# Optimization experiments

Hardware: AMD Instinct MI355X
Metric: run time of the kernel (lower is better)

The kernel has to match this reference:

```python
import jax, jax.numpy as jnp
import numpy as np
import math

EPS = 1e-5
NUM_HEADS = 8

def _ln(x, g, b):
    m = x.mean(-1, keepdims=True)
    v = ((x - m) ** 2).mean(-1, keepdims=True)
    return (x - m) / jnp.sqrt(v + EPS) * g + b

def _swish(x):
    return x * jax.nn.sigmoid(x)

def _rope(x):
    # lucidrains RotaryEmbedding.rotate_queries_or_keys: rotates along axis -2,
    # interleaved pair convention, base 10000.
    n, d = x.shape[-2], x.shape[-1]
    inv = 1.0 / (10000.0 ** (jnp.arange(0, d, 2, dtype=jnp.float32) / d))
    freqs = jnp.arange(n, dtype=jnp.float32)[:, None] * inv[None, :]  # (n, d/2)
    cos = jnp.repeat(jnp.cos(freqs), 2, axis=-1)  # (n, d)
    sin = jnp.repeat(jnp.sin(freqs), 2, axis=-1)
    x1, x2 = x[..., 0::2], x[..., 1::2]
    rot = jnp.stack([-x2, x1], axis=-1).reshape(x.shape)
    return x * cos + rot * sin

def _ffn(x, w1, b1, w2, b2):
    # FeedForwardModule: x + 0.5 * (Linear -> Swish -> Linear)
    return x + 0.5 * (_swish(x @ w1 + b1) @ w2 + b2)

def _mhsa(x, g, b, wq, bq, wk, bk, wv, bv, wo, bo):
    B, T, D = x.shape
    dh = D // NUM_HEADS
    y = _ln(x, g, b)
    q = (y @ wq + bq).reshape(B, T, NUM_HEADS, dh)                         # (b,t,h,d)
    k = (y @ wk + bk).reshape(B, T, NUM_HEADS, dh).transpose(0, 2, 1, 3)   # (b,h,t,d)
    v = (y @ wv + bv).reshape(B, T, NUM_HEADS, dh).transpose(0, 2, 1, 3)
    # Faithful to source: query is NOT permuted before rotary, so RoPE acts on
    # axis -2 which is heads for q and time for k (matches torch code exactly).
    q = _rope(q).transpose(0, 2, 1, 3)                                     # (b,h,t,d)
    k = _rope(k)
    score = jnp.einsum('bhtd,bhsd->bhts', q, k) / math.sqrt(D)             # /sqrt(d_model)
    attn = jax.nn.softmax(score, axis=-1)
    ctx = jnp.einsum('bhts,bhsd->bhtd', attn, v).transpose(0, 2, 1, 3).reshape(B, T, D)
    return x + ctx @ wo + bo

def _conv_module(x, g, b, pw1_w, pw1_b, dw_w, dw_b, bn_g, bn_b, pw2_w, pw2_b):
    C = dw_w.shape[-1]  # 2*dim
    y = _ln(x, g, b)
    y = jnp.einsum('btd,ed->bte', y, pw1_w) + pw1_b            # pointwise conv (b,t,4*dim)
    a, gate = y[..., :C], y[..., C:]
    y = a * jax.nn.sigmoid(gate)                                # GLU over channel dim
    y = jax.lax.conv_general_dilated(
        y, dw_w, window_strides=(1,), padding='SAME',
        dimension_numbers=('NWC', 'WIO', 'NWC'), feature_group_count=C) + dw_b
    m = y.mean(axis=(0, 1))                                     # BatchNorm1d, training stats
    v = ((y - m) ** 2).mean(axis=(0, 1))
    y = (y - m) / jnp.sqrt(v + EPS) * bn_g + bn_b
    y = _swish(y)
    y = jnp.einsum('btc,dc->btd', y, pw2_w) + pw2_b             # pointwise conv back to dim
    return x + y

def setup_inputs():
    key = jax.random.key(0)
    B, T, D, K = 8, 1024, 512, 31
    HID = 2 * D
    C = 2 * D
    ks = jax.random.split(key, 16)
    rn = lambda k, shp: jax.random.normal(k, shp, jnp.float32) * 0.02
    zeros = lambda n: jnp.zeros((n,), jnp.float32)
    ones = lambda n: jnp.ones((n,), jnp.float32)
    return dict(
        x=jax.random.normal(ks[0], (B, T, D), jnp.float32),
        ffn1_w1=rn(ks[1], (D, HID)), ffn1_b1=zeros(HID),
        ffn1_w2=rn(ks[2], (HID, D)), ffn1_b2=zeros(D),
        ln_attn_g=ones(D), ln_attn_b=zeros(D),
        wq=rn(ks[3], (D, D)), bq=zeros(D),
        wk=rn(ks[4], (D, D)), bk=zeros(D),
        wv=rn(ks[5], (D, D)), bv=zeros(D),
        wo=rn(ks[6], (D, D)), bo=zeros(D),
        conv_ln_g=ones(D), conv_ln_b=zeros(D),
        pw1_w=rn(ks[7], (2 * C, D)), pw1_b=zeros(2 * C),
        dw_w=rn(ks[8], (K, 1, C)), dw_b=zeros(C),
        bn_g=ones(C), bn_b=zeros(C),
        pw2_w=rn(ks[9], (D, C)), pw2_b=zeros(D),
        ffn2_w1=rn(ks[10], (D, HID)), ffn2_b1=zeros(HID),
        ffn2_w2=rn(ks[11], (HID, D)), ffn2_b2=zeros(D),
        ln_out_g=ones(D), ln_out_b=zeros(D),
    )

def reference(x, ffn1_w1, ffn1_b1, ffn1_w2, ffn1_b2, ln_attn_g, ln_attn_b,
              wq, bq, wk, bk, wv, bv, wo, bo,
              conv_ln_g, conv_ln_b, pw1_w, pw1_b, dw_w, dw_b, bn_g, bn_b, pw2_w, pw2_b,
              ffn2_w1, ffn2_b1, ffn2_w2, ffn2_b2, ln_out_g, ln_out_b):
    y = _ffn(x, ffn1_w1, ffn1_b1, ffn1_w2, ffn1_b2)
    y = _mhsa(y, ln_attn_g, ln_attn_b, wq, bq, wk, bk, wv, bv, wo, bo)
    y = _conv_module(y, conv_ln_g, conv_ln_b, pw1_w, pw1_b, dw_w, dw_b, bn_g, bn_b, pw2_w, pw2_b)
    y = _ffn(y, ffn2_w1, ffn2_b1, ffn2_w2, ffn2_b2)
    return _ln(y, ln_out_g, ln_out_b)
```

## Files before the change

### kernel.cpp

```cpp
#include <hip/hip_runtime.h>
#include <hip/hip_bf16.h>


#define M_ROWS 8192

using bf16x8 = __attribute__((ext_vector_type(8))) short;
using f32x4  = __attribute__((ext_vector_type(4))) float;
using s8v    = __attribute__((ext_vector_type(8))) short;
using s4v    = __attribute__((ext_vector_type(4))) short;

__device__ __forceinline__ float sigmoid_(float v) { return 1.f / (1.f + expf(-v)); }

__device__ __forceinline__ float bf2f(short s) {
  return __uint_as_float(((unsigned)(unsigned short)s) << 16);
}
__device__ __forceinline__ short f2bf(float f) {
  __hip_bfloat16 h = __float2bfloat16(f);
  return *reinterpret_cast<short*>(&h);
}

__device__ __forceinline__ void gl16(const void* g, void* l) {
  __builtin_amdgcn_global_load_lds((const __attribute__((address_space(1))) void*)g,
                                   (__attribute__((address_space(3))) void*)l, 16, 0, 0);
}

template <int BM, int BN, int BK, int EPI, int THREADS>
__global__ __launch_bounds__(THREADS) void mgemm(
    const short* __restrict__ A, const short* __restrict__ Bt,
    const float* __restrict__ bias, const float* __restrict__ res,
    const short* __restrict__ resb, short* __restrict__ outb, int M, int N, int K) {
  constexpr int NW = THREADS / 64;
  constexpr int WR = BM / 64;
  constexpr int WC = NW / WR;
  constexpr int NF = BN / (16 * WC);
  constexpr int CPW = BN / WC;
  constexpr int KH = BK / 32;
  constexpr int RPP = THREADS / (BK / 8);
  constexpr int APASS = BM / RPP;
  constexpr int BPASS = BN / RPP;
  constexpr int LPS = APASS + BPASS;
  __shared__ __align__(16) short smem[2 * BM * BK + 2 * BN * BK];
  short* As0 = smem;
  short* Bs0 = smem + 2 * BM * BK;
  const int tid = threadIdx.x;
  const int lane = tid & 63, wid = tid >> 6;
  const int wr = wid / WC, wc = wid % WC;
  const int nbx = gridDim.x;
  const int nwg = nbx * gridDim.y;
  int id = blockIdx.y * nbx + blockIdx.x;
  id = (id & 7) * (nwg >> 3) + (id >> 3);
  const int bm = (id / nbx) * BM;
  const int bn = (id % nbx) * BN;
  f32x4 acc[4][NF];
#pragma unroll
  for (int m = 0; m < 4; ++m)
#pragma unroll
    for (int n = 0; n < NF; ++n) acc[m][n] = (f32x4){0.f, 0.f, 0.f, 0.f};
  const short* Ablk = A + (size_t)bm * K;
  const short* Bblk = Bt + (size_t)bn * K;
  const int jl = tid & (BK / 8 - 1);
  const int r0 = tid / (BK / 8);
  const int ks = ((BK == 64) ? (jl ^ (r0 & 7)) : jl) << 3;
#define STAGE(buf, k0)                                                                 \
  do {                                                                                 \
    _Pragma("unroll")                                                                  \
    for (int p = 0; p < APASS; ++p)                                                    \
      gl16(Ablk + (size_t)(r0 + p * RPP) * K + (k0) + ks,                              \
           (char*)(As0 + (buf) * BM * BK) + p * (THREADS * 16) + wid * 1024);          \
    _Pragma("unroll")                                                                  \
    for (int p = 0; p < BPASS; ++p)                                                    \
      gl16(Bblk + (size_t)(r0 + p * RPP) * K + (k0) + ks,                              \
           (char*)(Bs0 + (buf) * BN * BK) + p * (THREADS * 16) + wid * 1024);          \
  } while (0)

  STAGE(0, 0);
  STAGE(1, BK);
  const int NS = K / BK;
  const int fr = lane & 15, fg = lane >> 4;
  const int arow = wr * 64 + fr;
  const int brow = wc * CPW + fr;
  for (int i = 0; i < NS; ++i) {
    if (i + 1 < NS) {
      if constexpr (LPS == 6)      asm volatile("s_waitcnt vmcnt(6)" ::: "memory");
      else if constexpr (LPS == 4) asm volatile("s_waitcnt vmcnt(4)" ::: "memory");
      else if constexpr (LPS == 3) asm volatile("s_waitcnt vmcnt(3)" ::: "memory");
      else                         asm volatile("s_waitcnt vmcnt(2)" ::: "memory");
    } else {
      asm volatile("s_waitcnt vmcnt(0)" ::: "memory");
    }
    __builtin_amdgcn_s_barrier();
    asm volatile("" ::: "memory");
    const int cur = i & 1;
    bf16x8 af[KH][4], bfr[KH][NF];
#pragma unroll
    for (int kk = 0; kk < KH; ++kk) {
      const int cx = (BK == 64) ? (((((kk << 2) + fg)) ^ (fr & 7)) << 3)
                                : ((fg << 3) + kk * 32);
#pragma unroll
      for (int m = 0; m < 4; ++m)
        af[kk][m] = *reinterpret_cast<const bf16x8*>(
            &As0[cur * BM * BK + (arow + m * 16) * BK + cx]);
#pragma unroll
      for (int n = 0; n < NF; ++n)
        bfr[kk][n] = *reinterpret_cast<const bf16x8*>(
            &Bs0[cur * BN * BK + (brow + n * 16) * BK + cx]);
    }
    asm volatile("s_waitcnt lgkmcnt(0)" ::: "memory");
    __builtin_amdgcn_s_barrier();
    if ((i + 2) * BK < K) STAGE(cur, (i + 2) * BK);
#pragma unroll
    for (int kk = 0; kk < KH; ++kk)
#pragma unroll
      for (int m = 0; m < 4; ++m)
#pragma unroll
        for (int n = 0; n < NF; ++n)
          acc[m][n] = __builtin_amdgcn_mfma_f32_16x16x32_bf16(af[kk][m], bfr[kk][n],
                                                              acc[m][n], 0, 0, 0);
  }
#undef STAGE
  const int orow0 = bm + wr * 64 + ((lane >> 4) << 2);
  const int ocol0 = bn + wc * CPW + fr;

  if constexpr (EPI == 4) {
    const int sel = bn >> 9;
    const float2* tbl = (const float2*)res;
    if (sel == 2) {
      short* vstg = smem;
      const int b_ = bm >> 10, t0v = bm & 1023;
      const int hb = (bn & 511) >> 6;
#pragma unroll
      for (int pass = 0; pass < 2; ++pass) {
        __syncthreads();
        if (((wc * CPW) >> 6) == pass) {
          const int dlb = (wc * CPW) & 63;
#pragma unroll
          for (int m = 0; m < 4; ++m) {
            const int rl = wr * 64 + ((lane >> 4) << 2) + m * 16;
#pragma unroll
            for (int n = 0; n < NF; ++n) {
              const int dl = dlb + n * 16 + fr;
              const float bv = bias[bn + pass * 64 + dl];
#pragma unroll
              for (int r = 0; r < 4; ++r)
                vstg[dl * 132 + rl + r] = f2bf(acc[m][n][r] + bv);
            }
          }
        }
        __syncthreads();
        for (int c = tid; c < 1024; c += THREADS) {
          const int d = c >> 4, t8 = (c & 15) << 3;
          const s8v val = *reinterpret_cast<const s8v*>(&vstg[d * 132 + t8]);
          *reinterpret_cast<s8v*>(
              &outb[(size_t)8388608 + (((size_t)((b_ << 3) + hb + pass)) << 16) +
                    ((size_t)d << 10) + t0v + t8]) = val;
        }
      }
    } else {
      const float qsc = (sel == 0) ? 0.04419417382415922f : 1.f;
#pragma unroll
      for (int n = 0; n < NF; ++n) {
        const int col = ocol0 + n * 16;
        const int h = (col >> 6) & 7, d = col & 63;
        const int p = d >> 1;
        const float bv = bias[col];
#pragma unroll
        for (int m = 0; m < 4; ++m) {
#pragma unroll
          for (int r = 0; r < 4; ++r) {
            const int row = orow0 + m * 16 + r;
            const int b_ = row >> 10, t_ = row & 1023;
            const int pos = (sel == 0) ? h : t_;
            const float2 cs = tbl[pos * 32 + p];
            float vv = acc[m][n][r] + bv;
            const float pv = __shfl_xor(vv, 1);
            float o = ((lane & 1) == 0) ? (vv * cs.x - pv * cs.y) : (vv * cs.x + pv * cs.y);
            outb[(size_t)sel * 4194304 + (((size_t)((b_ << 3) + h)) << 16) + ((size_t)t_ << 6) + d] =
                f2bf(o * qsc);
          }
        }
      }
    }
  } else if constexpr (EPI == 6) {
#pragma unroll
    for (int m = 0; m < 4; ++m) {
#pragma unroll
      for (int np = 0; np < NF / 2; ++np) {
        const int colbase = bn + wc * CPW + ((2 * np) << 4);
        const int j = colbase >> 7;
        const int u = (colbase >> 5) & 3;
        const int gc = (j << 6) + (u << 4) + fr;
        const float ba = bias[gc];
        const float bg = bias[1024 + gc];
#pragma unroll
        for (int r = 0; r < 4; ++r) {
          const int row = orow0 + m * 16 + r;
          const float a = acc[m][2 * np][r] + ba;
          const float g = acc[m][2 * np + 1][r] + bg;
          outb[(size_t)row * 1024 + gc] = f2bf(a * sigmoid_(g));
        }
      }
    }
  } else {
#pragma unroll
    for (int m = 0; m < 4; ++m) {
#pragma unroll
      for (int n = 0; n < NF; ++n) {
        const int col = ocol0 + n * 16;
        const float bv = bias[col];
#pragma unroll
        for (int r = 0; r < 4; ++r) {
          const int row = orow0 + m * 16 + r;
          float v = acc[m][n][r] + bv;
          if constexpr (EPI == 1) {
            v = v * sigmoid_(v);
          } else if constexpr (EPI == 2) {
            v += bf2f(resb[(size_t)row * N + col]);
          } else if constexpr (EPI == 3) {
            v = bf2f(resb[(size_t)row * N + col]) + 0.5f * v;
          }
          outb[(size_t)row * N + col] = f2bf(v);
        }
      }
    }
  }
}

__device__ __forceinline__ void dev_cast8(const float* in, short* out, int i) {
  const float4 a = *reinterpret_cast<const float4*>(&in[(size_t)i * 8]);
  const float4 b = *reinterpret_cast<const float4*>(&in[(size_t)i * 8 + 4]);
  s8v o = { f2bf(a.x), f2bf(a.y), f2bf(a.z), f2bf(a.w),
            f2bf(b.x), f2bf(b.y), f2bf(b.z), f2bf(b.w) };
  *reinterpret_cast<s8v*>(&out[(size_t)i * 8]) = o;
}

__global__ __launch_bounds__(256) void prep_kernel(
    const float* __restrict__ x, short* __restrict__ xb,
    const float* __restrict__ f1w1, short* __restrict__ wf1w1,
    const float* __restrict__ f1w2, short* __restrict__ wf1w2,
    const float* __restrict__ wq, const float* __restrict__ wk,
    const float* __restrict__ wv, short* __restrict__ wqkv,
    const float* __restrict__ wo, short* __restrict__ wwo,
    const float* __restrict__ pw1, short* __restrict__ wpw1,
    const float* __restrict__ pw2, short* __restrict__ wpw2,
    const float* __restrict__ f2w1, short* __restrict__ wf2w1,
    const float* __restrict__ f2w2, short* __restrict__ wf2w2,
    const float* __restrict__ bq, const float* __restrict__ bk,
    const float* __restrict__ bv, float* __restrict__ bqkv,
    float* __restrict__ rtbl) {
  __shared__ float t[32][33];
  const int blk = blockIdx.x, tid = threadIdx.x;
  const float* tin = nullptr;
  short* tout = nullptr;
  int tK = 0, tN = 0, tr = 0, tnbx = 0;
  if (blk < 2048) {
    dev_cast8(x, xb, blk * 256 + tid);
    return;
  } else if (blk < 2560) { tin = f1w1; tout = wf1w1; tK = 512; tN = 1024; tr = blk - 2048; tnbx = 32; }
  else if (blk < 3072)   { tin = f1w2; tout = wf1w2; tK = 1024; tN = 512; tr = blk - 2560; tnbx = 16; }
  else if (blk < 3328)   { tin = wq; tout = wqkv; tK = 512; tN = 512; tr = blk - 3072; tnbx = 16; }
  else if (blk < 3584)   { tin = wk; tout = wqkv + 512 * 512; tK = 512; tN = 512; tr = blk - 3328; tnbx = 16; }
  else if (blk < 3840)   { tin = wv; tout = wqkv + 1024 * 512; tK = 512; tN = 512; tr = blk - 3584; tnbx = 16; }
  else if (blk < 4096)   { tin = wo; tout = wwo; tK = 512; tN = 512; tr = blk - 3840; tnbx = 16; }
  else if (blk < 4608) {
    const int idx = (blk - 4096) * 256 + tid;
    const int pc = idx >> 6, kk = (idx & 63) << 3;
    const int j = pc >> 7, s = (pc >> 4) & 7, fr = pc & 15;
    const int oc = ((s & 1) << 10) + (j << 6) + ((s >> 1) << 4) + fr;
    const float4 a = *reinterpret_cast<const float4*>(&pw1[(size_t)oc * 512 + kk]);
    const float4 b = *reinterpret_cast<const float4*>(&pw1[(size_t)oc * 512 + kk + 4]);
    s8v o = { f2bf(a.x), f2bf(a.y), f2bf(a.z), f2bf(a.w),
              f2bf(b.x), f2bf(b.y), f2bf(b.z), f2bf(b.w) };
    *reinterpret_cast<s8v*>(&wpw1[(size_t)pc * 512 + kk]) = o;
    return;
  } else if (blk < 4864) {
    dev_cast8(pw2, wpw2, (blk - 4608) * 256 + tid);
    return;
  } else if (blk < 5376) { tin = f2w1; tout = wf2w1; tK = 512; tN = 1024; tr = blk - 4864; tnbx = 32; }
  else if (blk < 5888)   { tin = f2w2; tout = wf2w2; tK = 1024; tN = 512; tr = blk - 5376; tnbx = 16; }
  else if (blk < 6016) {
    const int i = (blk - 5888) * 256 + tid;
    const int tt = i >> 5, p = i & 31;
    const float inv = exp2f(-(float)p * 0.41524101186092f);
    float s, c;
    sincosf((float)tt * inv, &s, &c);
    rtbl[i * 2] = c;
    rtbl[i * 2 + 1] = s;
    return;
  } else {
    const int i = (blk - 6016) * 256 + tid;
    if (i < 1536) bqkv[i] = i < 512 ? bq[i] : (i < 1024 ? bk[i - 512] : bv[i - 1024]);
    return;
  }
  const int n0 = (tr % tnbx) << 5, k0 = (tr / tnbx) << 5;
  const int tx = tid & 31, ty = tid >> 5;
  for (int r = ty; r < 32; r += 8) t[r][tx] = tin[(size_t)(k0 + r) * tN + n0 + tx];
  __syncthreads();
  for (int r = ty; r < 32; r += 8) tout[(size_t)(n0 + r) * tK + k0 + tx] = f2bf(t[tx][r]);
}

template <typename OT>
__global__ __launch_bounds__(256) void ln_kernel(
    const short* __restrict__ in, const float* __restrict__ g,
    const float* __restrict__ b, OT* __restrict__ out) {
  const int tid = threadIdx.x, lane = tid & 63;
  const size_t row = ((size_t)blockIdx.x << 2) + (tid >> 6);
  const int c0 = lane << 3;
  const s8v v = *reinterpret_cast<const s8v*>(&in[(row << 9) + c0]);
  float f[8];
  float s = 0.f;
#pragma unroll
  for (int j = 0; j < 8; ++j) { f[j] = bf2f(v[j]); s += f[j]; }
  for (int o = 32; o; o >>= 1) s += __shfl_xor(s, o);
  const float mean = s * (1.f / 512.f);
  float d[8];
  float q = 0.f;
#pragma unroll
  for (int j = 0; j < 8; ++j) { d[j] = f[j] - mean; q = fmaf(d[j], d[j], q); }
  for (int o = 32; o; o >>= 1) q += __shfl_xor(q, o);
  const float inv = rsqrtf(q * (1.f / 512.f) + 1e-5f);
  const float4 g0 = *reinterpret_cast<const float4*>(&g[c0]);
  const float4 g1 = *reinterpret_cast<const float4*>(&g[c0 + 4]);
  const float4 b0 = *reinterpret_cast<const float4*>(&b[c0]);
  const float4 b1 = *reinterpret_cast<const float4*>(&b[c0 + 4]);
  const float gg[8] = {g0.x, g0.y, g0.z, g0.w, g1.x, g1.y, g1.z, g1.w};
  const float bb[8] = {b0.x, b0.y, b0.z, b0.w, b1.x, b1.y, b1.z, b1.w};
  if constexpr (sizeof(OT) == 2) {
    s8v o;
#pragma unroll
    for (int j = 0; j < 8; ++j) o[j] = f2bf(d[j] * inv * gg[j] + bb[j]);
    *reinterpret_cast<s8v*>(&out[(row << 9) + c0]) = o;
  } else {
    float4 o0, o1;
    o0.x = d[0] * inv * gg[0] + bb[0]; o0.y = d[1] * inv * gg[1] + bb[1];
    o0.z = d[2] * inv * gg[2] + bb[2]; o0.w = d[3] * inv * gg[3] + bb[3];
    o1.x = d[4] * inv * gg[4] + bb[4]; o1.y = d[5] * inv * gg[5] + bb[5];
    o1.z = d[6] * inv * gg[6] + bb[6]; o1.w = d[7] * inv * gg[7] + bb[7];
    *reinterpret_cast<float4*>(&out[(row << 9) + c0]) = o0;
    *reinterpret_cast<float4*>(&out[(row << 9) + c0 + 4]) = o1;
  }
}

__global__ __launch_bounds__(512) void attn_mfma_kernel(
    const short* __restrict__ q, const short* __restrict__ k,
    const short* __restrict__ vt, short* __restrict__ ctx) {
  __shared__ __align__(16) short Ks[2][64][72];
  __shared__ __align__(16) short VsT[2][64][72];
  __shared__ __align__(16) short Ps[2][64][72];
  const int bx = ((blockIdx.x & 7) << 6) | (blockIdx.x >> 3);
  const int bh = bx >> 3, qt = bx & 7;
  const int b_ = bh >> 3, h_ = bh & 7;
  const int tid = threadIdx.x, lane = tid & 63, w = tid >> 6;
  const int a = w >> 2, wl = w & 3;
  const int t0 = qt << 7;
  const short* qbase = q + ((size_t)bh << 16) + ((size_t)t0 << 6);
  const short* kbase = k + ((size_t)bh << 16);
  const short* vtbase = vt + ((size_t)bh << 16);
  const int sr = tid >> 3, sc = (tid & 7) << 3;
  short* Qtmp = &Ps[0][0][0];
  {
#pragma unroll
    for (int j = 0; j < 2; ++j) {
      const int idx = j * 512 + tid;
      const int qr_ = idx >> 3, qc = (idx & 7) << 3;
      const s8v v = *reinterpret_cast<const s8v*>(&qbase[(size_t)qr_ * 64 + qc]);
      *reinterpret_cast<s8v*>(&Qtmp[qr_ * 72 + qc]) = v;
    }
    const s8v k0v = *reinterpret_cast<const s8v*>(&kbase[(size_t)sr * 64 + sc]);
    *reinterpret_cast<s8v*>(&Ks[0][sr][sc]) = k0v;
    const s8v v0v = *reinterpret_cast<const s8v*>(&vtbase[((size_t)sr << 10) + sc]);
    *reinterpret_cast<s8v*>(&VsT[0][sr][sc]) = v0v;
  }
  __syncthreads();
  const int fr = lane & 15, fg = lane >> 4;
  const int koff0 = fg << 3;
  bf16x8 qf[2];
  qf[0] = *reinterpret_cast<const bf16x8*>(&Qtmp[(a * 64 + wl * 16 + fr) * 72 + koff0]);
  qf[1] = *reinterpret_cast<const bf16x8*>(&Qtmp[(a * 64 + wl * 16 + fr) * 72 + 32 + koff0]);
  __syncthreads();
  float m[4], l[4];
  f32x4 outv[4];
#pragma unroll
  for (int r = 0; r < 4; ++r) { m[r] = -1e30f; l[r] = 0.f; }
#pragma unroll
  for (int n = 0; n < 4; ++n) outv[n] = (f32x4){0.f, 0.f, 0.f, 0.f};

  for (int i = 0; i < 16; ++i) {
    const int cur = i & 1;
    s8v nk, nv;
    const bool pf = (i < 15);
    if (pf) {
      const int kn = (i + 1) << 6;
      nk = *reinterpret_cast<const s8v*>(&kbase[(size_t)(kn + sr) * 64 + sc]);
      nv = *reinterpret_cast<const s8v*>(&vtbase[((size_t)sr << 10) + kn + sc]);
    }
    f32x4 sacc[4];
    __builtin_amdgcn_s_setprio(1);
#pragma unroll
    for (int n = 0; n < 4; ++n) {
      const bf16x8 kf0 = *reinterpret_cast<const bf16x8*>(&Ks[cur][n * 16 + fr][koff0]);
      const bf16x8 kf1 = *reinterpret_cast<const bf16x8*>(&Ks[cur][n * 16 + fr][32 + koff0]);
      sacc[n] = (f32x4){0.f, 0.f, 0.f, 0.f};
      sacc[n] = __builtin_amdgcn_mfma_f32_16x16x32_bf16(qf[0], kf0, sacc[n], 0, 0, 0);
      sacc[n] = __builtin_amdgcn_mfma_f32_16x16x32_bf16(qf[1], kf1, sacc[n], 0, 0, 0);
    }
    __builtin_amdgcn_s_setprio(0);
    float vm[4];
    bool ok = true;
#pragma unroll
    for (int r = 0; r < 4; ++r) {
      vm[r] = fmaxf(fmaxf(sacc[0][r], sacc[1][r]), fmaxf(sacc[2][r], sacc[3][r]));
      ok = ok && (vm[r] <= m[r] + 8.f);
    }
    if (__all(ok)) {
#pragma unroll
      for (int r = 0; r < 4; ++r) {
        const float p0 = __expf(sacc[0][r] - m[r]), p1 = __expf(sacc[1][r] - m[r]);
        const float p2 = __expf(sacc[2][r] - m[r]), p3 = __expf(sacc[3][r] - m[r]);
        l[r] += p0 + p1 + p2 + p3;
        const int qr = wl * 16 + (fg << 2) + r;
        Ps[a][qr][fr] = f2bf(p0);
        Ps[a][qr][16 + fr] = f2bf(p1);
        Ps[a][qr][32 + fr] = f2bf(p2);
        Ps[a][qr][48 + fr] = f2bf(p3);
      }
    } else {
#pragma unroll
      for (int r = 0; r < 4; ++r) {
        float rm = vm[r];
        rm = fmaxf(rm, __shfl_xor(rm, 1));
        rm = fmaxf(rm, __shfl_xor(rm, 2));
        rm = fmaxf(rm, __shfl_xor(rm, 4));
        rm = fmaxf(rm, __shfl_xor(rm, 8));
        const float nm = fmaxf(m[r], rm);
        const float al = __expf(m[r] - nm);
        m[r] = nm;
        const float p0 = __expf(sacc[0][r] - nm), p1 = __expf(sacc[1][r] - nm);
        const float p2 = __expf(sacc[2][r] - nm), p3 = __expf(sacc[3][r] - nm);
        l[r] = l[r] * al + (p0 + p1 + p2 + p3);
        outv[0][r] *= al; outv[1][r] *= al; outv[2][r] *= al; outv[3][r] *= al;
        const int qr = wl * 16 + (fg << 2) + r;
        Ps[a][qr][fr] = f2bf(p0);
        Ps[a][qr][16 + fr] = f2bf(p1);
        Ps[a][qr][32 + fr] = f2bf(p2);
        Ps[a][qr][48 + fr] = f2bf(p3);
      }
    }
    __builtin_amdgcn_s_setprio(1);
    const bf16x8 pa0 = *reinterpret_cast<const bf16x8*>(&Ps[a][wl * 16 + fr][koff0]);
    const bf16x8 pa1 = *reinterpret_cast<const bf16x8*>(&Ps[a][wl * 16 + fr][32 + koff0]);
#pragma unroll
    for (int n = 0; n < 4; ++n) {
      const bf16x8 vf0 = *reinterpret_cast<const bf16x8*>(&VsT[cur][n * 16 + fr][koff0]);
      const bf16x8 vf1 = *reinterpret_cast<const bf16x8*>(&VsT[cur][n * 16 + fr][32 + koff0]);
      outv[n] = __builtin_amdgcn_mfma_f32_16x16x32_bf16(pa0, vf0, outv[n], 0, 0, 0);
      outv[n] = __builtin_amdgcn_mfma_f32_16x16x32_bf16(pa1, vf1, outv[n], 0, 0, 0);
    }
    __builtin_amdgcn_s_setprio(0);
    if (pf) {
      *reinterpret_cast<s8v*>(&Ks[cur ^ 1][sr][sc]) = nk;
      *reinterpret_cast<s8v*>(&VsT[cur ^ 1][sr][sc]) = nv;
    }
    __syncthreads();
  }
#pragma unroll
  for (int r = 0; r < 4; ++r) {
    float L = l[r];
    L += __shfl_xor(L, 1);
    L += __shfl_xor(L, 2);
    L += __shfl_xor(L, 4);
    L += __shfl_xor(L, 8);
    const float inv = 1.f / L;
    const int t = t0 + a * 64 + wl * 16 + (fg << 2) + r;
    const size_t base = (((size_t)((b_ << 10) | t)) << 9) + (h_ << 6);
#pragma unroll
    for (int n = 0; n < 4; ++n)
      ctx[base + n * 16 + fr] = f2bf(outv[n][r] * inv);
  }
}

__global__ __launch_bounds__(256) void dwconv_kernel(
    const short* __restrict__ in, const float* __restrict__ w,
    const float* __restrict__ bias, short* __restrict__ out,
    float* __restrict__ ps, float* __restrict__ pq) {
  __shared__ __align__(16) short tile[286 * 72];
  __shared__ float wlds[31 * 64];
  const int id = blockIdx.x;
  const int ct = id & 15, tt = (id >> 4) & 3;
  const size_t b = id >> 6;
  const int c0 = ct << 6, t0 = tt << 8;
  const int tid = threadIdx.x;
  for (int i = tid; i < 31 * 64; i += 256) {
    const int kk = i >> 6, c = i & 63;
    wlds[i] = w[kk * 1024 + c0 + c];
  }
  for (int i = tid; i < 286 * 8; i += 256) {
    const int row = i >> 3, seg = i & 7;
    const int gt = t0 - 15 + row;
    s8v val = {};
    if (gt >= 0 && gt < 1024)
      val = *reinterpret_cast<const s8v*>(&in[(b << 20) + ((size_t)gt << 10) + c0 + (seg << 3)]);
    *reinterpret_cast<s8v*>(&tile[row * 72 + (seg << 3)]) = val;
  }
  __syncthreads();
  const int cg = tid & 7, tg = tid >> 3;
  const int tl = tg << 3;
  float acc[8][8];
  const float4 b0 = *reinterpret_cast<const float4*>(&bias[c0 + (cg << 3)]);
  const float4 b1 = *reinterpret_cast<const float4*>(&bias[c0 + (cg << 3) + 4]);
#pragma unroll
  for (int t = 0; t < 8; ++t) {
    acc[t][0] = b0.x; acc[t][1] = b0.y; acc[t][2] = b0.z; acc[t][3] = b0.w;
    acc[t][4] = b1.x; acc[t][5] = b1.y; acc[t][6] = b1.z; acc[t][7] = b1.w;
  }
  for (int kk = 0; kk < 31; ++kk) {
    const float4 w0 = *reinterpret_cast<const float4*>(&wlds[kk * 64 + (cg << 3)]);
    const float4 w1 = *reinterpret_cast<const float4*>(&wlds[kk * 64 + (cg << 3) + 4]);
#pragma unroll
    for (int t = 0; t < 8; ++t) {
      const s8v xv = *reinterpret_cast<const s8v*>(&tile[(tl + t + kk) * 72 + (cg << 3)]);
      acc[t][0] = fmaf(bf2f(xv[0]), w0.x, acc[t][0]);
      acc[t][1] = fmaf(bf2f(xv[1]), w0.y, acc[t][1]);
      acc[t][2] = fmaf(bf2f(xv[2]), w0.z, acc[t][2]);
      acc[t][3] = fmaf(bf2f(xv[3]), w0.w, acc[t][3]);
      acc[t][4] = fmaf(bf2f(xv[4]), w1.x, acc[t][4]);
      acc[t][5] = fmaf(bf2f(xv[5]), w1.y, acc[t][5]);
      acc[t][6] = fmaf(bf2f(xv[6]), w1.z, acc[t][6]);
      acc[t][7] = fmaf(bf2f(xv[7]), w1.w, acc[t][7]);
    }
  }
#pragma unroll
  for (int t = 0; t < 8; ++t) {
    s8v o;
#pragma unroll
    for (int j = 0; j < 8; ++j) o[j] = f2bf(acc[t][j]);
    *reinterpret_cast<s8v*>(&out[(b << 20) + ((size_t)(t0 + tl + t) << 10) + c0 + (cg << 3)]) = o;
  }
  float s8_[8], q8_[8];
#pragma unroll
  for (int j = 0; j < 8; ++j) {
    float S = 0.f, Q = 0.f;
#pragma unroll
    for (int t = 0; t < 8; ++t) {
      S += acc[t][j];
      Q = fmaf(acc[t][j], acc[t][j], Q);
    }
    s8_[j] = S;
    q8_[j] = Q;
  }
  __syncthreads();
  float* fred = (float*)tile;
#pragma unroll
  for (int j = 0; j < 8; ++j) {
    fred[tid * 16 + j] = s8_[j];
    fred[tid * 16 + 8 + j] = q8_[j];
  }
  __syncthreads();
  if (tid < 64) {
    const int cg_ = tid >> 3, j_ = tid & 7;
    float S = 0.f, Q = 0.f;
    for (int tg_ = 0; tg_ < 32; ++tg_) {
      const int th = tg_ * 8 + cg_;
      S += fred[th * 16 + j_];
      Q += fred[th * 16 + 8 + j_];
    }
    const int pidx = ((int)b << 2) + tt;
    ps[pidx * 1024 + c0 + tid] = S;
    pq[pidx * 1024 + c0 + tid] = Q;
  }
}

__global__ __launch_bounds__(256) void bn_finalize_kernel(
    const float* __restrict__ ps, const float* __restrict__ pq, float* __restrict__ stats) {
  const int c = blockIdx.x * 256 + threadIdx.x;
  float s = 0.f, q = 0.f;
  for (int i = 0; i < 32; ++i) {
    s += ps[i * 1024 + c];
    q += pq[i * 1024 + c];
  }
  const float mean = s * (1.f / 8192.f);
  const float var = q * (1.f / 8192.f) - mean * mean;
  stats[c] = mean;
  stats[1024 + c] = rsqrtf(fmaxf(var, 0.f) + 1e-5f);
}

__global__ __launch_bounds__(256) void bn_apply_kernel(
    const short* __restrict__ y, const float* __restrict__ g, const float* __restrict__ b,
    const float* __restrict__ stats, short* __restrict__ out) {
  const size_t i = (size_t)blockIdx.x * 256 + threadIdx.x;
  const size_t f = i << 2;
  const int c = (int)(f & 1023);
  const s4v yv = *reinterpret_cast<const s4v*>(&y[f]);
  s4v o;
#pragma unroll
  for (int j = 0; j < 4; ++j) {
    const float v = (bf2f(yv[j]) - stats[c + j]) * stats[1024 + c + j] * g[c + j] + b[c + j];
    o[j] = f2bf(v * sigmoid_(v));
  }
  *reinterpret_cast<s4v*>(&out[f]) = o;
}

extern "C" void kernel_launch(void* const* d_in, const int* in_sizes, int n_in,
                              void* d_out, int out_size, void* d_ws, size_t ws_size,
                              hipStream_t stream) {
  const float* x        = (const float*)d_in[0];
  const float* ffn1_w1  = (const float*)d_in[1];
  const float* ffn1_b1  = (const float*)d_in[2];
  const float* ffn1_w2  = (const float*)d_in[3];
  const float* ffn1_b2  = (const float*)d_in[4];
  const float* ln_att_g = (const float*)d_in[5];
  const float* ln_att_b = (const float*)d_in[6];
  const float* wq       = (const float*)d_in[7];
  const float* bq       = (const float*)d_in[8];
  const float* wk       = (const float*)d_in[9];
  const float* bk       = (const float*)d_in[10];
  const float* wv       = (const float*)d_in[11];
  const float* bv       = (const float*)d_in[12];
  const float* wo_      = (const float*)d_in[13];
  const float* bo       = (const float*)d_in[14];
  const float* cln_g    = (const float*)d_in[15];
  const float* cln_b    = (const float*)d_in[16];
  const float* pw1_w    = (const float*)d_in[17];
  const float* pw1_b    = (const float*)d_in[18];
  const float* dw_w     = (const float*)d_in[19];
  const float* dw_b     = (const float*)d_in[20];
  const float* bn_g     = (const float*)d_in[21];
  const float* bn_b     = (const float*)d_in[22];
  const float* pw2_w    = (const float*)d_in[23];
  const float* pw2_b    = (const float*)d_in[24];
  const float* ffn2_w1  = (const float*)d_in[25];
  const float* ffn2_b1  = (const float*)d_in[26];
  const float* ffn2_w2  = (const float*)d_in[27];
  const float* ffn2_b2  = (const float*)d_in[28];
  const float* ln_out_g = (const float*)d_in[29];
  const float* ln_out_b = (const float*)d_in[30];

  char* wsb = (char*)d_ws;
  const size_t MB = 1u << 20;
  short* buf_y = (short*)(wsb);
  char* Bre = wsb + 16 * MB;
  short* qkv16 = (short*)(Bre);
  short* lnq  = (short*)(Bre + 48 * MB);
  short* ctx  = (short*)(Bre + 56 * MB);
  short* h1   = (short*)(Bre);
  short* xb   = (short*)(Bre + 16 * MB);
  short* gluo = (short*)(Bre);
  short* bno  = (short*)(Bre + 48 * MB);
  char* Cre = wsb + 80 * MB;
  short* lnc  = (short*)(Cre);
  short* dwo16= (short*)(Cre + 8 * MB);
  char* Dre = wsb + 112 * MB;
  short* w_f1w1 = (short*)(Dre);
  short* w_f1w2 = (short*)(Dre + 1 * MB);
  short* w_qkv  = (short*)(Dre + 2 * MB);
  short* w_wo   = (short*)(Dre + 3 * MB + 512 * 1024);
  short* w_pw1  = (short*)(Dre + 4 * MB);
  short* w_pw2  = (short*)(Dre + 6 * MB);
  short* w_f2w1 = (short*)(Dre + 7 * MB);
  short* w_f2w2 = (short*)(Dre + 8 * MB);
  float* bqkv   = (float*)(Dre + 9 * MB);
  float* ps     = (float*)(Dre + 9 * MB + 8192);
  float* pq     = (float*)(Dre + 10 * MB + 8192);
  float* stats  = (float*)(Dre + 11 * MB + 8192);
  float* rtbl   = (float*)(Dre + 12 * MB);

  const dim3 blk(256);

  prep_kernel<<<6022, blk, 0, stream>>>(
      x, xb, ffn1_w1, w_f1w1, ffn1_w2, w_f1w2, wq, wk, wv, w_qkv, wo_, w_wo,
      pw1_w, w_pw1, pw2_w, w_pw2, ffn2_w1, w_f2w1, ffn2_w2, w_f2w2,
      bq, bk, bv, bqkv, rtbl);

  mgemm<64, 128, 64, 1, 512><<<dim3(8, 128), dim3(512), 0, stream>>>(xb, w_f1w1, ffn1_b1, nullptr, nullptr, h1, M_ROWS, 1024, 512);
  mgemm<64, 128, 64, 3, 512><<<dim3(4, 128), dim3(512), 0, stream>>>(h1, w_f1w2, ffn1_b2, nullptr, xb, buf_y, M_ROWS, 512, 1024);

  ln_kernel<short><<<2048, blk, 0, stream>>>(buf_y, ln_att_g, ln_att_b, lnq);
  mgemm<128, 128, 32, 4, 512><<<dim3(12, 64), dim3(512), 0, stream>>>(lnq, w_qkv, bqkv, rtbl, nullptr, qkv16, M_ROWS, 1536, 512);
  attn_mfma_kernel<<<512, dim3(512), 0, stream>>>(qkv16, qkv16 + 4194304, qkv16 + 8388608, ctx);
  mgemm<64, 128, 64, 2, 512><<<dim3(4, 128), dim3(512), 0, stream>>>(ctx, w_wo, bo, nullptr, buf_y, buf_y, M_ROWS, 512, 512);

  ln_kernel<short><<<2048, blk, 0, stream>>>(buf_y, cln_g, cln_b, lnc);
  mgemm<128, 256, 32, 6, 512><<<dim3(8, 64), dim3(512), 0, stream>>>(lnc, w_pw1, pw1_b, nullptr, nullptr, gluo, M_ROWS, 2048, 512);
  dwconv_kernel<<<512, blk, 0, stream>>>(gluo, dw_w, dw_b, dwo16, ps, pq);
  bn_finalize_kernel<<<4, blk, 0, stream>>>(ps, pq, stats);
  bn_apply_kernel<<<8192, blk, 0, stream>>>(dwo16, bn_g, bn_b, stats, bno);
  mgemm<64, 128, 64, 2, 512><<<dim3(4, 128), dim3(512), 0, stream>>>(bno, w_pw2, pw2_b, nullptr, buf_y, buf_y, M_ROWS, 512, 1024);

  mgemm<64, 128, 64, 1, 512><<<dim3(8, 128), dim3(512), 0, stream>>>(buf_y, w_f2w1, ffn2_b1, nullptr, nullptr, h1, M_ROWS, 1024, 512);
  mgemm<64, 128, 64, 3, 512><<<dim3(4, 128), dim3(512), 0, stream>>>(h1, w_f2w2, ffn2_b2, nullptr, buf_y, buf_y, M_ROWS, 512, 1024);

  ln_kernel<float><<<2048, blk, 0, stream>>>(buf_y, ln_out_g, ln_out_b, (float*)d_out);
}
```

Baseline: 244.6 us.

## Split attention over key halves with a separate combine kernel

The attention kernel now splits each query tile's key range into two halves, doubling the grid from 512 to 1024 blocks. Each half writes unnormalized fp32 partial outputs plus per-row max and sum to workspace, and a new combine kernel merges them into bf16 ctx. To reduce LDS, K/V staging drops from double to single buffering, with an extra barrier per iteration. The goal is better CU occupancy and load balance, at the cost of extra global traffic for the partials, another launch and more synchronisation.

Measured after the change: 255.5 us. 4.5% more time.

```diff
diff --git a/kernel.cpp b/kernel.cpp
--- a/kernel.cpp
+++ b/kernel.cpp
@@ -342,19 +342,18 @@
 
 __global__ __launch_bounds__(512) void attn_mfma_kernel(
     const short* __restrict__ q, const short* __restrict__ k,
-    const short* __restrict__ vt, short* __restrict__ ctx) {
-  __shared__ __align__(16) short Ks[2][64][72];
-  __shared__ __align__(16) short VsT[2][64][72];
+    const short* __restrict__ vt, float* __restrict__ pO, float2* __restrict__ ml) {
+  __shared__ __align__(16) short Ks[64][72];
+  __shared__ __align__(16) short VsT[64][72];
   __shared__ __align__(16) short Ps[2][64][72];
-  const int bx = ((blockIdx.x & 7) << 6) | (blockIdx.x >> 3);
-  const int bh = bx >> 3, qt = bx & 7;
-  const int b_ = bh >> 3, h_ = bh & 7;
+  const int bx = ((blockIdx.x & 7) << 7) | (blockIdx.x >> 3);
+  const int qt = bx & 7, half = (bx >> 3) & 1, bh = bx >> 4;
   const int tid = threadIdx.x, lane = tid & 63, w = tid >> 6;
   const int a = w >> 2, wl = w & 3;
   const int t0 = qt << 7;
   const short* qbase = q + ((size_t)bh << 16) + ((size_t)t0 << 6);
-  const short* kbase = k + ((size_t)bh << 16);
-  const short* vtbase = vt + ((size_t)bh << 16);
+  const short* kbase = k + ((size_t)bh << 16) + ((size_t)(half * 512) << 6);
+  const short* vtbase = vt + ((size_t)bh << 16) + half * 512;
   const int sr = tid >> 3, sc = (tid & 7) << 3;
   short* Qtmp = &Ps[0][0][0];
   {
@@ -366,9 +365,9 @@
       *reinterpret_cast<s8v*>(&Qtmp[qr_ * 72 + qc]) = v;
     }
     const s8v k0v = *reinterpret_cast<const s8v*>(&kbase[(size_t)sr * 64 + sc]);
-    *reinterpret_cast<s8v*>(&Ks[0][sr][sc]) = k0v;
+    *reinterpret_cast<s8v*>(&Ks[sr][sc]) = k0v;
     const s8v v0v = *reinterpret_cast<const s8v*>(&vtbase[((size_t)sr << 10) + sc]);
-    *reinterpret_cast<s8v*>(&VsT[0][sr][sc]) = v0v;
+    *reinterpret_cast<s8v*>(&VsT[sr][sc]) = v0v;
   }
   __syncthreads();
   const int fr = lane & 15, fg = lane >> 4;
@@ -384,10 +383,9 @@
 #pragma unroll
   for (int n = 0; n < 4; ++n) outv[n] = (f32x4){0.f, 0.f, 0.f, 0.f};
 
-  for (int i = 0; i < 16; ++i) {
-    const int cur = i & 1;
+  for (int i = 0; i < 8; ++i) {
     s8v nk, nv;
-    const bool pf = (i < 15);
+    const bool pf = (i < 7);
     if (pf) {
       const int kn = (i + 1) << 6;
       nk = *reinterpret_cast<const s8v*>(&kbase[(size_t)(kn + sr) * 64 + sc]);
@@ -397,8 +395,8 @@
     __builtin_amdgcn_s_setprio(1);
 #pragma unroll
     for (int n = 0; n < 4; ++n) {
-      const bf16x8 kf0 = *reinterpret_cast<const bf16x8*>(&Ks[cur][n * 16 + fr][koff0]);
-      const bf16x8 kf1 = *reinterpret_cast<const bf16x8*>(&Ks[cur][n * 16 + fr][32 + koff0]);
+      const bf16x8 kf0 = *reinterpret_cast<const bf16x8*>(&Ks[n * 16 + fr][koff0]);
+      const bf16x8 kf1 = *reinterpret_cast<const bf16x8*>(&Ks[n * 16 + fr][32 + koff0]);
       sacc[n] = (f32x4){0.f, 0.f, 0.f, 0.f};
       sacc[n] = __builtin_amdgcn_mfma_f32_16x16x32_bf16(qf[0], kf0, sacc[n], 0, 0, 0);
       sacc[n] = __builtin_amdgcn_mfma_f32_16x16x32_bf16(qf[1], kf1, sacc[n], 0, 0, 0);
@@ -445,22 +443,25 @@
         Ps[a][qr][48 + fr] = f2bf(p3);
       }
     }
+    __syncthreads();
+    if (pf) {
+      *reinterpret_cast<s8v*>(&Ks[sr][sc]) = nk;
+    }
     __builtin_amdgcn_s_setprio(1);
     const bf16x8 pa0 = *reinterpret_cast<const bf16x8*>(&Ps[a][wl * 16 + fr][koff0]);
     const bf16x8 pa1 = *reinterpret_cast<const bf16x8*>(&Ps[a][wl * 16 + fr][32 + koff0]);
 #pragma unroll
     for (int n = 0; n < 4; ++n) {
-      const bf16x8 vf0 = *reinterpret_cast<const bf16x8*>(&VsT[cur][n * 16 + fr][koff0]);
-      const bf16x8 vf1 = *reinterpret_cast<const bf16x8*>(&VsT[cur][n * 16 + fr][32 + koff0]);
+      const bf16x8 vf0 = *reinterpret_cast<const bf16x8*>(&VsT[n * 16 + fr][koff0]);
+      const bf16x8 vf1 = *reinterpret_cast<const bf16x8*>(&VsT[n * 16 + fr][32 + koff0]);
       outv[n] = __builtin_amdgcn_mfma_f32_16x16x32_bf16(pa0, vf0, outv[n], 0, 0, 0);
       outv[n] = __builtin_amdgcn_mfma_f32_16x16x32_bf16(pa1, vf1, outv[n], 0, 0, 0);
     }
     __builtin_amdgcn_s_setprio(0);
+    __syncthreads();
     if (pf) {
-      *reinterpret_cast<s8v*>(&Ks[cur ^ 1][sr][sc]) = nk;
-      *reinterpret_cast<s8v*>(&VsT[cur ^ 1][sr][sc]) = nv;
-    }
-    __syncthreads();
+      *reinterpret_cast<s8v*>(&VsT[sr][sc]) = nv;
+    }
   }
 #pragma unroll
   for (int r = 0; r < 4; ++r) {
@@ -469,13 +470,35 @@
     L += __shfl_xor(L, 2);
     L += __shfl_xor(L, 4);
     L += __shfl_xor(L, 8);
-    const float inv = 1.f / L;
-    const int t = t0 + a * 64 + wl * 16 + (fg << 2) + r;
-    const size_t base = (((size_t)((b_ << 10) | t)) << 9) + (h_ << 6);
+    const int trow = t0 + a * 64 + wl * 16 + (fg << 2) + r;
+    const size_t base = (size_t)half * 4194304 + ((size_t)bh << 16) + (size_t)trow * 64;
 #pragma unroll
     for (int n = 0; n < 4; ++n)
-      ctx[base + n * 16 + fr] = f2bf(outv[n][r] * inv);
-  }
+      pO[base + n * 16 + fr] = outv[n][r];
+    if (fr == 0)
+      ml[half * 65536 + (bh << 10) + trow] = make_float2(m[r], L);
+  }
+}
+
+__global__ __launch_bounds__(256) void attn_combine_kernel(
+    const float* __restrict__ pO, const float2* __restrict__ ml,
+    short* __restrict__ ctx) {
+  const int g = blockIdx.x * 256 + threadIdx.x;
+  const int row = g >> 4, dq = (g & 15) << 2;
+  const float2 ml0 = ml[row];
+  const float2 ml1 = ml[65536 + row];
+  const float M = fmaxf(ml0.x, ml1.x);
+  const float a0 = __expf(ml0.x - M), a1 = __expf(ml1.x - M);
+  const float inv = 1.f / (ml0.y * a0 + ml1.y * a1);
+  const float4 o0 = *reinterpret_cast<const float4*>(&pO[(size_t)row * 64 + dq]);
+  const float4 o1 = *reinterpret_cast<const float4*>(&pO[4194304 + (size_t)row * 64 + dq]);
+  const int b = row >> 13, h = (row >> 10) & 7, t = row & 1023;
+  s4v o;
+  o[0] = f2bf((o0.x * a0 + o1.x * a1) * inv);
+  o[1] = f2bf((o0.y * a0 + o1.y * a1) * inv);
+  o[2] = f2bf((o0.z * a0 + o1.z * a1) * inv);
+  o[3] = f2bf((o0.w * a0 + o1.w * a1) * inv);
+  *reinterpret_cast<s4v*>(&ctx[(((size_t)((b << 10) | t)) << 9) + (h << 6) + dq]) = o;
 }
 
 __global__ __launch_bounds__(256) void dwconv_kernel(
@@ -648,6 +671,7 @@
   char* Cre = wsb + 80 * MB;
   short* lnc  = (short*)(Cre);
   short* dwo16= (short*)(Cre + 8 * MB);
+  float* pO   = (float*)(Cre);
   char* Dre = wsb + 112 * MB;
   short* w_f1w1 = (short*)(Dre);
   short* w_f1w2 = (short*)(Dre + 1 * MB);
@@ -662,6 +686,7 @@
   float* pq     = (float*)(Dre + 10 * MB + 8192);
   float* stats  = (float*)(Dre + 11 * MB + 8192);
   float* rtbl   = (float*)(Dre + 12 * MB);
+  float2* ml    = (float2*)(Dre + 13 * MB);
 
   const dim3 blk(256);
 
@@ -675,7 +700,8 @@
 
   ln_kernel<short><<<2048, blk, 0, stream>>>(buf_y, ln_att_g, ln_att_b, lnq);
   mgemm<128, 128, 32, 4, 512><<<dim3(12, 64), dim3(512), 0, stream>>>(lnq, w_qkv, bqkv, rtbl, nullptr, qkv16, M_ROWS, 1536, 512);
-  attn_mfma_kernel<<<512, dim3(512), 0, stream>>>(qkv16, qkv16 + 4194304, qkv16 + 8388608, ctx);
+  attn_mfma_kernel<<<1024, dim3(512), 0, stream>>>(qkv16, qkv16 + 4194304, qkv16 + 8388608, pO, ml);
+  attn_combine_kernel<<<4096, blk, 0, stream>>>(pO, ml, ctx);
   mgemm<64, 128, 64, 2, 512><<<dim3(4, 128), dim3(512), 0, stream>>>(ctx, w_wo, bo, nullptr, buf_y, buf_y, M_ROWS, 512, 512);
 
   ln_kernel<short><<<2048, blk, 0, stream>>>(buf_y, cln_g, cln_b, lnc);
```
